# Kernel tuning notes

Hardware: AMD Instinct MI355X
Metric: run time of the kernel (lower is better)

Reference implementation:

```python
import jax, jax.numpy as jnp
import numpy as np

N, E, D, G, L = 100000, 1600000, 64, 512, 3
EPS = 1e-5


def setup_inputs() -> dict:
    key = jax.random.key(0)
    ks = jax.random.split(key, 8)
    x = jax.random.normal(ks[0], (N, D), dtype=jnp.float32)
    edge_index = jax.random.randint(ks[1], (2, E), 0, N, dtype=jnp.int32)
    batch = jnp.sort(jax.random.randint(ks[2], (N,), 0, G, dtype=jnp.int32))
    s = 1.0 / np.sqrt(D)
    convW = jax.random.normal(ks[3], (L, D, D), dtype=jnp.float32) * s
    convB = jnp.zeros((L, D), jnp.float32)
    bn_g = jnp.ones((L, D), jnp.float32); bn_b = jnp.zeros((L, D), jnp.float32)
    ln_g = jnp.ones((L, D), jnp.float32); ln_b = jnp.zeros((L, D), jnp.float32)
    W1 = jax.random.normal(ks[4], (3 * D, 2 * D), dtype=jnp.float32) * (1.0 / np.sqrt(3 * D))
    b1 = jnp.zeros((2 * D,), jnp.float32)
    ln1_g = jnp.ones((2 * D,), jnp.float32); ln1_b = jnp.zeros((2 * D,), jnp.float32)
    W2 = jax.random.normal(ks[5], (2 * D, D), dtype=jnp.float32) * (1.0 / np.sqrt(2 * D))
    b2 = jnp.zeros((D,), jnp.float32)
    ln2_g = jnp.ones((D,), jnp.float32); ln2_b = jnp.zeros((D,), jnp.float32)
    W3 = jax.random.normal(ks[6], (D, 1), dtype=jnp.float32) * s
    b3 = jnp.zeros((1,), jnp.float32)
    return dict(x=x, edge_index=edge_index, batch=batch, convW=convW, convB=convB,
                bn_g=bn_g, bn_b=bn_b, ln_g=ln_g, ln_b=ln_b,
                W1=W1, b1=b1, ln1_g=ln1_g, ln1_b=ln1_b,
                W2=W2, b2=b2, ln2_g=ln2_g, ln2_b=ln2_b, W3=W3, b3=b3)


def _layer_norm(h, g, b):
    mu = jnp.mean(h, axis=-1, keepdims=True)
    var = jnp.mean((h - mu) ** 2, axis=-1, keepdims=True)
    return (h - mu) * jax.lax.rsqrt(var + EPS) * g + b


def _forward(x, edge_index, batch, convW, convB, bn_g, bn_b, ln_g, ln_b,
             W1, b1, ln1_g, ln1_b, W2, b2, ln2_g, ln2_b, W3, b3):
    n = x.shape[0]
    loops = jnp.arange(n, dtype=edge_index.dtype)
    src = jnp.concatenate([edge_index[0], loops])  # self-loops as in GCNConv
    dst = jnp.concatenate([edge_index[1], loops])
    deg = jax.ops.segment_sum(jnp.ones_like(src, dtype=x.dtype), dst, num_segments=n)
    dinv = jnp.where(deg > 0, jax.lax.rsqrt(deg), 0.0)
    norm = (dinv[src] * dinv[dst])[:, None]  # [E+N, 1]

    h = x
    for i in range(L):
        x_in = h
        hw = h @ convW[i]                                   # [N, D]
        agg = jax.ops.segment_sum(norm * hw[src], dst, num_segments=n) + convB[i]
        # BatchNorm1d (train-mode batch stats, biased var)
        mu = jnp.mean(agg, axis=0)
        var = jnp.mean((agg - mu) ** 2, axis=0)
        hb = (agg - mu) * jax.lax.rsqrt(var + EPS) * bn_g[i] + bn_b[i]
        if i > 0:
            hb = hb + x_in  # residual (shapes match: D == D)
        h = jax.nn.gelu(_layer_norm(hb, ln_g[i], ln_b[i]), approximate=False)

    # multi-pool over graphs
    cnt = jax.ops.segment_sum(jnp.ones((n,), x.dtype), batch, num_segments=G)[:, None]
    s = jax.ops.segment_sum(h, batch, num_segments=G)
    mean = s / jnp.maximum(cnt, 1.0)
    mx = jax.ops.segment_max(h, batch, num_segments=G)
    mx = jnp.where(cnt > 0, mx, 0.0)
    z = jnp.concatenate([mean, mx, s], axis=1)  # [G, 3D]

    z = jax.nn.gelu(_layer_norm(z @ W1 + b1, ln1_g, ln1_b), approximate=False)
    z = jax.nn.gelu(_layer_norm(z @ W2 + b2, ln2_g, ln2_b), approximate=False)
    return z @ W3 + b3  # [G, num_classes]


def reference(x, edge_index, batch, convW, convB, bn_g, bn_b, ln_g, ln_b,
              W1, b1, ln1_g, ln1_b, W2, b2, ln2_g, ln2_b, W3, b3):
    return _forward(x, edge_index, batch, convW, convB, bn_g, bn_b, ln_g, ln_b,
                    W1, b1, ln1_g, ln1_b, W2, b2, ln2_g, ln2_b, W3, b3)
```

## Files before the change

kernel.cpp:

```cpp
#include <hip/hip_runtime.h>
#include <hip/hip_bf16.h>
#include <hip/hip_fp16.h>

#define DD 64
#define EPSV 1e-5f
#define NSLICE 16

typedef __attribute__((ext_vector_type(4))) _Float16 f16x4;
typedef __attribute__((ext_vector_type(8))) _Float16 f16x8;
typedef __attribute__((ext_vector_type(4))) float f32x4;

static __device__ __forceinline__ float fatomic_add(float* p, float v) {
#if defined(__HIP_DEVICE_COMPILE__)
    return unsafeAtomicAdd(p, v);
#else
    return 0.f;
#endif
}

static __device__ __forceinline__ float gelu_exact(float x) {
    return 0.5f * x * (1.0f + erff(x * 0.70710678118654752f));
}

static __device__ __forceinline__ void acc_u4(float* a8, uint4 v) {
    const __half2* hp = reinterpret_cast<const __half2*>(&v);
#pragma unroll
    for (int p = 0; p < 4; ++p) {
        float2 f = __half22float2(hp[p]);
        a8[2 * p] += f.x;
        a8[2 * p + 1] += f.y;
    }
}

__global__ void k_hist(const int* __restrict__ dst, int* __restrict__ counts, int e) {
    int i = blockIdx.x * 256 + threadIdx.x;
    if (i < e) atomicAdd(&counts[dst[i]], 1);
}

__global__ __launch_bounds__(1024) void k_bsum(const int* __restrict__ counts,
                                               int* __restrict__ bsum, int n) {
    __shared__ int wsum[16];
    int t = threadIdx.x;
    int i = blockIdx.x * 1024 + t;
    int v = (i < n) ? counts[i] : 0;
    int lane = t & 63, wv = t >> 6;
    int x = v;
#pragma unroll
    for (int o = 1; o < 64; o <<= 1) x += __shfl_xor(x, o, 64);
    if (lane == 0) wsum[wv] = x;
    __syncthreads();
    if (t == 0) {
        int r = 0;
#pragma unroll
        for (int w = 0; w < 16; ++w) r += wsum[w];
        bsum[blockIdx.x] = r;
    }
}

__global__ __launch_bounds__(128) void k_bscan(int* __restrict__ bsum, int nb) {
    __shared__ int ws[2];
    int t = threadIdx.x;
    int lane = t & 63, wv = t >> 6;
    int v = (t < nb) ? bsum[t] : 0;
    int x = v;
#pragma unroll
    for (int o = 1; o < 64; o <<= 1) {
        int u = __shfl_up(x, o, 64);
        if (lane >= o) x += u;
    }
    if (lane == 63) ws[wv] = x;
    __syncthreads();
    int add = (wv == 1) ? ws[0] : 0;
    if (t < nb) bsum[t] = add + x - v;
}

__global__ __launch_bounds__(1024) void k_downsweep(const int* __restrict__ counts,
                                                    const int* __restrict__ bsum,
                                                    int* __restrict__ off,
                                                    float* __restrict__ dinv,
                                                    int* __restrict__ bcur,
                                                    int n, int etotal) {
    __shared__ int wsum[16];
    int t = threadIdx.x;
    int i = blockIdx.x * 1024 + t;
    int v = (i < n) ? counts[i] : 0;
    int lane = t & 63, wv = t >> 6;
    int x = v;
#pragma unroll
    for (int o = 1; o < 64; o <<= 1) {
        int u = __shfl_up(x, o, 64);
        if (lane >= o) x += u;
    }
    if (lane == 63) wsum[wv] = x;
    __syncthreads();
    if (t == 0) {
        int r = 0;
#pragma unroll
        for (int w = 0; w < 16; ++w) { int y = wsum[w]; wsum[w] = r; r += y; }
    }
    __syncthreads();
    if (i < n) {
        int excl = bsum[blockIdx.x] + wsum[wv] + x - v;
        off[i] = excl;
        dinv[i] = rsqrtf((float)v + 1.0f);
        if ((i & 255) == 0) bcur[i >> 8] = excl;
        if (i == n - 1) off[n] = etotal;
    }
}

__global__ __launch_bounds__(1024) void k_dhist(const int* __restrict__ off,
                                                int* __restrict__ dcount, int n) {
    __shared__ int h[256];
    int t = threadIdx.x;
    if (t < 256) h[t] = 0;
    __syncthreads();
    int i = blockIdx.x * 1024 + t;
    if (i < n) {
        int d = min(off[i + 1] - off[i], 255);
        atomicAdd(&h[d], 1);
    }
    __syncthreads();
    if (t < 256 && h[t]) atomicAdd(&dcount[t], h[t]);
}

__global__ __launch_bounds__(256) void k_dscan(const int* __restrict__ dcount,
                                               int* __restrict__ dcur) {
    __shared__ int ws[4];
    int t = threadIdx.x;
    int lane = t & 63, wv = t >> 6;
    int v = dcount[t];
    int x = v;
#pragma unroll
    for (int o = 1; o < 64; o <<= 1) {
        int u = __shfl_up(x, o, 64);
        if (lane >= o) x += u;
    }
    if (lane == 63) ws[wv] = x;
    __syncthreads();
    int add = 0;
    for (int w = 0; w < wv; ++w) add += ws[w];
    dcur[t] = add + x - v;
}

__global__ __launch_bounds__(1024) void k_dscatter(const int* __restrict__ off,
                                                   int* __restrict__ dcur,
                                                   int* __restrict__ perm, int n) {
    __shared__ int lcnt[256], lbase[256];
    int t = threadIdx.x;
    if (t < 256) lcnt[t] = 0;
    __syncthreads();
    int i = blockIdx.x * 1024 + t;
    int d = 0, rank = 0;
    if (i < n) {
        d = min(off[i + 1] - off[i], 255);
        rank = atomicAdd(&lcnt[d], 1);
    }
    __syncthreads();
    if (t < 256 && lcnt[t]) lbase[t] = atomicAdd(&dcur[t], lcnt[t]);
    __syncthreads();
    if (i < n) perm[lbase[d] + rank] = i;
}

#define ACHUNK 2048
#define NBMAX 400
__global__ __launch_bounds__(256) void k_binA(const int* __restrict__ src,
                                              const int* __restrict__ dst,
                                              int* __restrict__ ebuf,
                                              int* __restrict__ bcur,
                                              int e, int nbuck) {
    __shared__ int cnt[NBMAX], startb[NBMAX], posb[NBMAX], gbase[NBMAX];
    __shared__ int stage[ACHUNK];
    __shared__ unsigned short stb[ACHUNK];
    int t = threadIdx.x;
    for (int cbase = blockIdx.x * ACHUNK; cbase < e; cbase += gridDim.x * ACHUNK) {
        int cval = min(ACHUNK, e - cbase);
        for (int i = t; i < nbuck; i += 256) { cnt[i] = 0; posb[i] = 0; }
        __syncthreads();
        int eb[8], es[8];
#pragma unroll
        for (int k = 0; k < 8; ++k) {
            int i = t + k * 256;
            if (i < cval) {
                int s = src[cbase + i];
                int d = dst[cbase + i];
                eb[k] = d >> 8;
                es[k] = s | ((d & 255) << 24);
                atomicAdd(&cnt[eb[k]], 1);
            } else eb[k] = -1;
        }
        __syncthreads();
        if (t == 0) {
            int r = 0;
            for (int b2 = 0; b2 < nbuck; ++b2) { startb[b2] = r; r += cnt[b2]; }
        }
        __syncthreads();
        for (int i = t; i < nbuck; i += 256)
            if (cnt[i] > 0) gbase[i] = atomicAdd(&bcur[i], cnt[i]);
#pragma unroll
        for (int k = 0; k < 8; ++k)
            if (eb[k] >= 0) {
                int idx = startb[eb[k]] + atomicAdd(&posb[eb[k]], 1);
                stage[idx] = es[k];
                stb[idx] = (unsigned short)eb[k];
            }
        __syncthreads();
        for (int i = t; i < cval; i += 256) {
            int b2 = stb[i];
            ebuf[gbase[b2] + (i - startb[b2])] = stage[i];
        }
        __syncthreads();
    }
}

__global__ __launch_bounds__(256) void k_binB(const int* __restrict__ ebuf,
                                              const int* __restrict__ offs,
                                              int* __restrict__ csr, int n) {
    __shared__ int cur[256];
    int b = blockIdx.x;
    int base = b << 8;
    int nn = min(256, n - base);
    int t = threadIdx.x;
    if (t < nn) cur[t] = offs[base + t];
    __syncthreads();
    int e0 = offs[base], e1 = offs[base + nn];
    for (int i = e0 + t; i < e1; i += 256) {
        int packed = ebuf[i];
        int dl = ((unsigned)packed) >> 24;
        int pos = atomicAdd(&cur[dl], 1);
        csr[pos] = packed & 0x00FFFFFF;
    }
}

__global__ void k_misc(const float* __restrict__ x, const float* __restrict__ dinv,
                       __half* __restrict__ mA, __half* __restrict__ mB, int n,
                       const int* __restrict__ batch, int* __restrict__ bnd, int g) {
    int i = blockIdx.x * 256 + threadIdx.x;
    int total = n * 64;
    if (i < total) {
        mA[i] = __float2half_rn(x[i] * dinv[i >> 6]);
    } else if (i < total + 64) {
        mA[i] = __float2half_rn(0.f);
        mB[i] = __float2half_rn(0.f);
    }
    if (i < n) {
        int b = batch[i];
        if (i == 0)
            for (int q = 0; q <= b; ++q) bnd[q] = 0;
        else {
            int pb = batch[i - 1];
            for (int q = pb + 1; q <= b; ++q) bnd[q] = i;
        }
        if (i == n - 1)
            for (int q = b + 1; q <= g; ++q) bnd[q] = n;
    }
}

__global__ __launch_bounds__(256, 4) void k_gather_gemm(const int* __restrict__ off,
                                                        const int* __restrict__ csr,
                                                        const float* __restrict__ dinv,
                                                        const __half* __restrict__ m16,
                                                        const float* __restrict__ W,
                                                        const float* __restrict__ convB,
                                                        const int* __restrict__ perm,
                                                        float* __restrict__ agg,
                                                        float* __restrict__ gstat,
                                                        int n, int nzero) {
    __shared__ float sred[128];
    const int t = threadIdx.x;
    const int lane = t & 63, wv = t >> 6;
    const int g = lane >> 4, ln = lane & 15;

    f16x8 bfr[2][4];
#pragma unroll
    for (int kt = 0; kt < 2; ++kt)
#pragma unroll
        for (int nt = 0; nt < 4; ++nt) {
            f16x8 h;
#pragma unroll
            for (int j = 0; j < 8; ++j)
                h[j] = (_Float16)W[(32 * kt + 8 * g + j) * 64 + 16 * nt + ln];
            bfr[kt][nt] = h;
        }

    if (t < 128) sred[t] = 0.f;
    __syncthreads();

    const int ntiles = (n + 15) >> 4;
    const int tile = blockIdx.x * 4 + wv;
    float s_acc[4] = {0.f, 0.f, 0.f, 0.f}, q_acc[4] = {0.f, 0.f, 0.f, 0.f};

    if (tile < ntiles) {
        const int slot = tile * 16 + ln;
        const bool valid = slot < n;
        const int node = valid ? perm[slot] : -1;
        const int row_self = valid ? node : nzero;
        int a = 0, deg = 0;
        float dd = 0.f;
        if (valid) {
            a = off[node];
            deg = off[node + 1] - a;
            dd = dinv[node];
        }
        int md = deg;
#pragma unroll
        for (int o = 1; o < 64; o <<= 1) md = max(md, __shfl_xor(md, o, 64));

        float acc[2][8];
#pragma unroll
        for (int kt = 0; kt < 2; ++kt)
#pragma unroll
            for (int j = 0; j < 8; ++j) acc[kt][j] = 0.f;

        const uint4* mrow4 = (const uint4*)m16;
        {
            const uint4* rp = mrow4 + ((size_t)row_self << 3) + g;
            uint4 v0 = rp[0], v1 = rp[4];
            acc_u4(acc[0], v0);
            acc_u4(acc[1], v1);
        }
        int ecur[4];
#pragma unroll
        for (int k = 0; k < 4; ++k) ecur[k] = (k < deg) ? csr[a + k] : nzero;
        for (int i = 0; i < md; i += 4) {
            int enx[4];
#pragma unroll
            for (int k = 0; k < 4; ++k) enx[k] = (i + 4 + k < deg) ? csr[a + i + 4 + k] : nzero;
            uint4 v[4][2];
#pragma unroll
            for (int r = 0; r < 4; ++r) {
                const uint4* rp = mrow4 + ((size_t)ecur[r] << 3) + g;
                v[r][0] = rp[0];
                v[r][1] = rp[4];
            }
#pragma unroll
            for (int r = 0; r < 4; ++r) {
                acc_u4(acc[0], v[r][0]);
                acc_u4(acc[1], v[r][1]);
            }
#pragma unroll
            for (int k = 0; k < 4; ++k) ecur[k] = enx[k];
        }

        f32x4 c[4];
#pragma unroll
        for (int nt = 0; nt < 4; ++nt) c[nt] = (f32x4){0.f, 0.f, 0.f, 0.f};
#pragma unroll
        for (int kt = 0; kt < 2; ++kt) {
            f16x8 ah, ar;
#pragma unroll
            for (int j = 0; j < 8; ++j) {
                float v = acc[kt][j] * dd;
                _Float16 h = (_Float16)v;
                ah[j] = h;
                ar[j] = (_Float16)(v - (float)h);
            }
#pragma unroll
            for (int nt = 0; nt < 4; ++nt) {
                c[nt] = __builtin_amdgcn_mfma_f32_16x16x32_f16(ah, bfr[kt][nt], c[nt], 0, 0, 0);
                c[nt] = __builtin_amdgcn_mfma_f32_16x16x32_f16(ar, bfr[kt][nt], c[nt], 0, 0, 0);
            }
        }

        int prow[4];
#pragma unroll
        for (int i = 0; i < 4; ++i) prow[i] = __shfl(node, 4 * g + i, 64);
        const float bias[4] = {convB[ln], convB[16 + ln], convB[32 + ln], convB[48 + ln]};
#pragma unroll
        for (int nt = 0; nt < 4; ++nt) {
#pragma unroll
            for (int i = 0; i < 4; ++i) {
                if (prow[i] >= 0) {
                    float v = c[nt][i] + bias[nt];
                    agg[(size_t)prow[i] * 64 + 16 * nt + ln] = v;
                    s_acc[nt] += v;
                    q_acc[nt] += v * v;
                }
            }
        }
#pragma unroll
        for (int nt = 0; nt < 4; ++nt) {
            s_acc[nt] += __shfl_xor(s_acc[nt], 16, 64);
            s_acc[nt] += __shfl_xor(s_acc[nt], 32, 64);
            q_acc[nt] += __shfl_xor(q_acc[nt], 16, 64);
            q_acc[nt] += __shfl_xor(q_acc[nt], 32, 64);
        }
        if (g == 0) {
#pragma unroll
            for (int nt = 0; nt < 4; ++nt) {
                atomicAdd(&sred[16 * nt + ln], s_acc[nt]);
                atomicAdd(&sred[64 + 16 * nt + ln], q_acc[nt]);
            }
        }
    }
    __syncthreads();
    if (t < 64) {
        float* gs = gstat + (blockIdx.x & (NSLICE - 1)) * 128;
        fatomic_add(&gs[t], sred[t]);
        fatomic_add(&gs[64 + t], sred[64 + t]);
    }
}

__global__ __launch_bounds__(256) void k_bn_ln_gelu(const float* __restrict__ agg,
                                                    const __half* __restrict__ m16res,
                                                    const float* __restrict__ gstat,
                                                    const float* __restrict__ dinv,
                                                    const float* __restrict__ bng,
                                                    const float* __restrict__ bnb,
                                                    const float* __restrict__ lng,
                                                    const float* __restrict__ lnb,
                                                    __half* __restrict__ m16out,
                                                    int n, int has_res, int scale_out) {
    int t = threadIdx.x;
    int lane = t & 63, wv = t >> 6;
    float fs = 0.f, fq = 0.f;
#pragma unroll
    for (int s = 0; s < NSLICE; ++s) {
        fs += gstat[s * 128 + lane];
        fq += gstat[s * 128 + 64 + lane];
    }
    float invN = 1.0f / (float)n;
    float mu_c = fs * invN;
    float var_c = fq * invN - mu_c * mu_c;
    float bscale = rsqrtf(var_c + EPSV) * bng[lane];
    float bshift = bnb[lane];
    float lg = lng[lane], lb = lnb[lane];
    for (int r = blockIdx.x * 4 + wv; r < n; r += gridDim.x * 4) {
        float dd = dinv[r];
        float x = agg[(size_t)r * 64 + lane];
        float hb = (x - mu_c) * bscale + bshift;
        if (has_res) hb += __half2float(m16res[(size_t)r * 64 + lane]) * (1.0f / dd);
        float ssum = hb;
#pragma unroll
        for (int off = 32; off; off >>= 1) ssum += __shfl_xor(ssum, off, 64);
        float rmu = ssum * (1.f / 64.f);
        float d = hb - rmu;
        float vs = d * d;
#pragma unroll
        for (int off = 32; off; off >>= 1) vs += __shfl_xor(vs, off, 64);
        float rvar = vs * (1.f / 64.f);
        float ln = d * rsqrtf(rvar + EPSV) * lg + lb;
        float g = gelu_exact(ln);
        float outv = scale_out ? g * dd : g;
        m16out[(size_t)r * 64 + lane] = __float2half_rn(outv);
    }
}

__global__ __launch_bounds__(256) void k_pool_z(const __half* __restrict__ h,
                                                const int* __restrict__ bnd,
                                                float* __restrict__ z) {
    int g = blockIdx.x;
    int t = threadIdx.x;
    int lane = t & 63, wv = t >> 6;
    int s0 = bnd[g], e0 = bnd[g + 1];
    float s = 0.f, mx = -INFINITY;
    for (int i = s0 + wv; i < e0; i += 4) {
        float v = __half2float(h[(size_t)i * 64 + lane]);
        s += v;
        mx = fmaxf(mx, v);
    }
    __shared__ float ss[256], sm[256];
    ss[t] = s;
    sm[t] = mx;
    __syncthreads();
    if (t < 64) {
        float fs = ss[t] + ss[t + 64] + ss[t + 128] + ss[t + 192];
        float fm = fmaxf(fmaxf(sm[t], sm[t + 64]), fmaxf(sm[t + 128], sm[t + 192]));
        float cntf = (float)(e0 - s0);
        float mean = fs / fmaxf(cntf, 1.0f);
        if (e0 == s0) fm = 0.f;
        z[g * 192 + t] = mean;
        z[g * 192 + 64 + t] = fm;
        z[g * 192 + 128 + t] = fs;
    }
}

__global__ __launch_bounds__(128) void k_head(const float* __restrict__ z,
                                              const float* __restrict__ W1, const float* __restrict__ b1,
                                              const float* __restrict__ ln1g, const float* __restrict__ ln1b,
                                              const float* __restrict__ W2, const float* __restrict__ b2,
                                              const float* __restrict__ ln2g, const float* __restrict__ ln2b,
                                              const float* __restrict__ W3, const float* __restrict__ b3,
                                              float* __restrict__ out) {
    int g = blockIdx.x;
    int t = threadIdx.x;
    int lane = t & 63, wv = t >> 6;
    __shared__ float zl[192], h1[128], red[2];
    for (int i = t; i < 192; i += 128) zl[i] = z[g * 192 + i];
    __syncthreads();
    float acc = b1[t];
    for (int k = 0; k < 192; ++k) acc += zl[k] * W1[k * 128 + t];
    float s = acc;
#pragma unroll
    for (int off = 32; off; off >>= 1) s += __shfl_xor(s, off, 64);
    if (lane == 0) red[wv] = s;
    __syncthreads();
    float mu = (red[0] + red[1]) * (1.f / 128.f);
    float d = acc - mu;
    float q = d * d;
#pragma unroll
    for (int off = 32; off; off >>= 1) q += __shfl_xor(q, off, 64);
    __syncthreads();
    if (lane == 0) red[wv] = q;
    __syncthreads();
    float var = (red[0] + red[1]) * (1.f / 128.f);
    float ln = d * rsqrtf(var + EPSV) * ln1g[t] + ln1b[t];
    h1[t] = gelu_exact(ln);
    __syncthreads();
    if (t < 64) {
        float acc2 = b2[t];
        for (int k = 0; k < 128; ++k) acc2 += h1[k] * W2[k * 64 + t];
        float s2 = acc2;
#pragma unroll
        for (int off = 32; off; off >>= 1) s2 += __shfl_xor(s2, off, 64);
        float mu2 = s2 * (1.f / 64.f);
        float d2 = acc2 - mu2;
        float q2 = d2 * d2;
#pragma unroll
        for (int off = 32; off; off >>= 1) q2 += __shfl_xor(q2, off, 64);
        float var2 = q2 * (1.f / 64.f);
        float l2 = d2 * rsqrtf(var2 + EPSV) * ln2g[t] + ln2b[t];
        float g2 = gelu_exact(l2);
        float p = g2 * W3[t];
#pragma unroll
        for (int off = 32; off; off >>= 1) p += __shfl_xor(p, off, 64);
        if (t == 0) out[g] = p + b3[0];
    }
}

extern "C" void kernel_launch(void* const* d_in, const int* in_sizes, int n_in,
                              void* d_out, int out_size, void* d_ws, size_t ws_size,
                              hipStream_t stream) {
    const float* x      = (const float*)d_in[0];
    const int*   eidx   = (const int*)d_in[1];
    const int*   batch  = (const int*)d_in[2];
    const float* convW  = (const float*)d_in[3];
    const float* convB  = (const float*)d_in[4];
    const float* bn_g   = (const float*)d_in[5];
    const float* bn_b   = (const float*)d_in[6];
    const float* ln_g   = (const float*)d_in[7];
    const float* ln_b   = (const float*)d_in[8];
    const float* W1     = (const float*)d_in[9];
    const float* b1     = (const float*)d_in[10];
    const float* ln1g   = (const float*)d_in[11];
    const float* ln1b   = (const float*)d_in[12];
    const float* W2     = (const float*)d_in[13];
    const float* b2     = (const float*)d_in[14];
    const float* ln2g   = (const float*)d_in[15];
    const float* ln2b   = (const float*)d_in[16];
    const float* W3     = (const float*)d_in[17];
    const float* b3     = (const float*)d_in[18];
    float* out = (float*)d_out;

    const int N = in_sizes[0] / DD;
    const int E = in_sizes[1] / 2;
    const int G = out_size;
    const int* esrc = eidx;
    const int* edst = eidx + E;

    char* ws = (char*)d_ws;
    size_t off_b = 0;
    auto alloc = [&](size_t bytes) {
        size_t p = off_b;
        off_b = (off_b + bytes + 255) & ~(size_t)255;
        return (void*)(ws + p);
    };
    int*    offs   = (int*)alloc((size_t)(N + 1) * 4);
    float*  dinv   = (float*)alloc((size_t)N * 4);
    int*    csr    = (int*)alloc((size_t)E * 4);
    int*    ebuf   = (int*)alloc((size_t)E * 4);
    __half* m16A   = (__half*)alloc((size_t)(N + 1) * DD * 2);
    __half* m16B   = (__half*)alloc((size_t)(N + 1) * DD * 2);
    float*  aggbuf = (float*)alloc((size_t)N * DD * 4);
    float*  gstats = (float*)alloc((size_t)3 * NSLICE * 128 * 4);
    int*    perm   = (int*)alloc((size_t)N * 4);
    int*    dcount = (int*)alloc(256 * 4);
    int*    dcur   = (int*)alloc(256 * 4);
    int*    bnd    = (int*)alloc((size_t)(G + 1) * 4);
    int*    bsum   = (int*)alloc(((size_t)(N + 1023) / 1024) * 4);
    int*    bcur   = (int*)alloc(((size_t)(N + 255) / 256) * 4);
    int*   counts = (int*)aggbuf;
    float* z      = aggbuf;
    (void)ws_size; (void)n_in;

    const int nb = (N + 1023) / 1024;
    const int nbuck = (N + 255) / 256;

    hipMemsetAsync(counts, 0, (size_t)N * 4, stream);
    hipMemsetAsync(gstats, 0, (size_t)3 * NSLICE * 128 * 4, stream);
    hipMemsetAsync(dcount, 0, 256 * 4, stream);
    k_hist<<<(E + 255) / 256, 256, 0, stream>>>(edst, counts, E);
    k_bsum<<<nb, 1024, 0, stream>>>(counts, bsum, N);
    k_bscan<<<1, 128, 0, stream>>>(bsum, nb);
    k_downsweep<<<nb, 1024, 0, stream>>>(counts, bsum, offs, dinv, bcur, N, E);
    k_dhist<<<nb, 1024, 0, stream>>>(offs, dcount, N);
    k_dscan<<<1, 256, 0, stream>>>(dcount, dcur);
    k_dscatter<<<nb, 1024, 0, stream>>>(offs, dcur, perm, N);
    k_binA<<<(E + ACHUNK - 1) / ACHUNK, 256, 0, stream>>>(esrc, edst, ebuf, bcur, E, nbuck);
    k_binB<<<nbuck, 256, 0, stream>>>(ebuf, offs, csr, N);
    k_misc<<<((N + 1) * DD + 255) / 256, 256, 0, stream>>>(x, dinv, m16A, m16B, N, batch, bnd, G);

    __half* gin[3]  = {m16A, m16B, m16A};
    __half* gout[3] = {m16B, m16A, m16B};

    const int ntiles = (N + 15) / 16;
    const int gblocks = (ntiles + 3) / 4;

    for (int l = 0; l < 3; ++l) {
        float* gstat = gstats + (size_t)l * NSLICE * 128;
        k_gather_gemm<<<gblocks, 256, 0, stream>>>(offs, csr, dinv, (const __half*)gin[l],
                                                   convW + (size_t)l * DD * DD, convB + l * DD,
                                                   perm, aggbuf, gstat, N, N);
        k_bn_ln_gelu<<<2048, 256, 0, stream>>>(aggbuf, gin[l], gstat, dinv,
                                               bn_g + l * DD, bn_b + l * DD,
                                               ln_g + l * DD, ln_b + l * DD,
                                               gout[l], N, l > 0 ? 1 : 0, l < 2 ? 1 : 0);
    }

    k_pool_z<<<G, 256, 0, stream>>>(m16B, bnd, z);
    k_head<<<G, 128, 0, stream>>>(z, W1, b1, ln1g, ln1b, W2, b2, ln2g, ln2b, W3, b3, out);
}
```

Baseline: 476.6 us.

## Build CSR from bucket-level counts and compute per-node offsets inside binB

Replaces the per-node global degree histogram with a bucket-level histogram done in shared memory, followed by a single-block scan over buckets. Per-node offsets and dinv are now computed inside k_binB with a local count and scan over each bucket's edges. This removes the N-sized memset, the 1.6M global atomics on node counters and two scan kernels. The cost is an extra pass over ebuf in binB, and the degree-sort kernels are moved after binB because they depend on offs.

```diff
diff --git a/kernel.cpp b/kernel.cpp
--- a/kernel.cpp
+++ b/kernel.cpp
@@ -32,36 +32,35 @@
     }
 }
 
-__global__ void k_hist(const int* __restrict__ dst, int* __restrict__ counts, int e) {
-    int i = blockIdx.x * 256 + threadIdx.x;
-    if (i < e) atomicAdd(&counts[dst[i]], 1);
-}
-
-__global__ __launch_bounds__(1024) void k_bsum(const int* __restrict__ counts,
-                                               int* __restrict__ bsum, int n) {
-    __shared__ int wsum[16];
-    int t = threadIdx.x;
-    int i = blockIdx.x * 1024 + t;
-    int v = (i < n) ? counts[i] : 0;
-    int lane = t & 63, wv = t >> 6;
-    int x = v;
-#pragma unroll
-    for (int o = 1; o < 64; o <<= 1) x += __shfl_xor(x, o, 64);
-    if (lane == 0) wsum[wv] = x;
-    __syncthreads();
-    if (t == 0) {
-        int r = 0;
-#pragma unroll
-        for (int w = 0; w < 16; ++w) r += wsum[w];
-        bsum[blockIdx.x] = r;
-    }
-}
-
-__global__ __launch_bounds__(128) void k_bscan(int* __restrict__ bsum, int nb) {
-    __shared__ int ws[2];
-    int t = threadIdx.x;
-    int lane = t & 63, wv = t >> 6;
-    int v = (t < nb) ? bsum[t] : 0;
+#define ACHUNK 2048
+#define NBMAX 400
+
+__global__ __launch_bounds__(1024) void k_bcount(const int* __restrict__ dst,
+                                                 int* __restrict__ bucketCnt,
+                                                 int e, int nbuck) {
+    __shared__ int h[NBMAX];
+    int t = threadIdx.x;
+    for (int i = t; i < nbuck; i += 1024) h[i] = 0;
+    __syncthreads();
+    int base = blockIdx.x * 8192;
+#pragma unroll
+    for (int k = 0; k < 8; ++k) {
+        int i = base + k * 1024 + t;
+        if (i < e) atomicAdd(&h[dst[i] >> 8], 1);
+    }
+    __syncthreads();
+    for (int i = t; i < nbuck; i += 1024)
+        if (h[i]) atomicAdd(&bucketCnt[i], h[i]);
+}
+
+__global__ __launch_bounds__(512) void k_bscan2(const int* __restrict__ bucketCnt,
+                                                int* __restrict__ bbase,
+                                                int* __restrict__ bcur,
+                                                int* __restrict__ offs,
+                                                int nbuck, int etotal, int n) {
+    __shared__ int ws[8];
+    int t = threadIdx.x, lane = t & 63, wv = t >> 6;
+    int v = (t < nbuck) ? bucketCnt[t] : 0;
     int x = v;
 #pragma unroll
     for (int o = 1; o < 64; o <<= 1) {
@@ -70,41 +69,16 @@
     }
     if (lane == 63) ws[wv] = x;
     __syncthreads();
-    int add = (wv == 1) ? ws[0] : 0;
-    if (t < nb) bsum[t] = add + x - v;
-}
-
-__global__ __launch_bounds__(1024) void k_downsweep(const int* __restrict__ counts,
-                                                    const int* __restrict__ bsum,
-                                                    int* __restrict__ off,
-                                                    float* __restrict__ dinv,
-                                                    int* __restrict__ bcur,
-                                                    int n, int etotal) {
-    __shared__ int wsum[16];
-    int t = threadIdx.x;
-    int i = blockIdx.x * 1024 + t;
-    int v = (i < n) ? counts[i] : 0;
-    int lane = t & 63, wv = t >> 6;
-    int x = v;
-#pragma unroll
-    for (int o = 1; o < 64; o <<= 1) {
-        int u = __shfl_up(x, o, 64);
-        if (lane >= o) x += u;
-    }
-    if (lane == 63) wsum[wv] = x;
-    __syncthreads();
+    int add = 0;
+    for (int w = 0; w < wv; ++w) add += ws[w];
+    int excl = add + x - v;
+    if (t < nbuck) {
+        bbase[t] = excl;
+        bcur[t] = excl;
+    }
     if (t == 0) {
-        int r = 0;
-#pragma unroll
-        for (int w = 0; w < 16; ++w) { int y = wsum[w]; wsum[w] = r; r += y; }
-    }
-    __syncthreads();
-    if (i < n) {
-        int excl = bsum[blockIdx.x] + wsum[wv] + x - v;
-        off[i] = excl;
-        dinv[i] = rsqrtf((float)v + 1.0f);
-        if ((i & 255) == 0) bcur[i >> 8] = excl;
-        if (i == n - 1) off[n] = etotal;
+        bbase[nbuck] = etotal;
+        offs[n] = etotal;
     }
 }
 
@@ -161,8 +135,6 @@
     if (i < n) perm[lbase[d] + rank] = i;
 }
 
-#define ACHUNK 2048
-#define NBMAX 400
 __global__ __launch_bounds__(256) void k_binA(const int* __restrict__ src,
                                               const int* __restrict__ dst,
                                               int* __restrict__ ebuf,
@@ -213,16 +185,40 @@
 }
 
 __global__ __launch_bounds__(256) void k_binB(const int* __restrict__ ebuf,
-                                              const int* __restrict__ offs,
+                                              const int* __restrict__ bbase,
+                                              int* __restrict__ offs,
+                                              float* __restrict__ dinv,
                                               int* __restrict__ csr, int n) {
-    __shared__ int cur[256];
+    __shared__ int cnt[256], cur[256], ws[4];
     int b = blockIdx.x;
     int base = b << 8;
     int nn = min(256, n - base);
     int t = threadIdx.x;
-    if (t < nn) cur[t] = offs[base + t];
-    __syncthreads();
-    int e0 = offs[base], e1 = offs[base + nn];
+    int e0 = bbase[b], e1 = bbase[b + 1];
+    cnt[t] = 0;
+    __syncthreads();
+    for (int i = e0 + t; i < e1; i += 256)
+        atomicAdd(&cnt[((unsigned)ebuf[i]) >> 24], 1);
+    __syncthreads();
+    int v = cnt[t];
+    int lane = t & 63, wv = t >> 6;
+    int x = v;
+#pragma unroll
+    for (int o = 1; o < 64; o <<= 1) {
+        int u = __shfl_up(x, o, 64);
+        if (lane >= o) x += u;
+    }
+    if (lane == 63) ws[wv] = x;
+    __syncthreads();
+    int add = 0;
+    for (int w = 0; w < wv; ++w) add += ws[w];
+    int excl = add + x - v;
+    if (t < nn) {
+        offs[base + t] = e0 + excl;
+        dinv[base + t] = rsqrtf((float)v + 1.0f);
+    }
+    cur[t] = e0 + excl;
+    __syncthreads();
     for (int i = e0 + t; i < e1; i += 256) {
         int packed = ebuf[i];
         int dl = ((unsigned)packed) >> 24;
@@ -576,27 +572,25 @@
     int*    dcount = (int*)alloc(256 * 4);
     int*    dcur   = (int*)alloc(256 * 4);
     int*    bnd    = (int*)alloc((size_t)(G + 1) * 4);
-    int*    bsum   = (int*)alloc(((size_t)(N + 1023) / 1024) * 4);
+    int*    bucketCnt = (int*)alloc((size_t)NBMAX * 4);
+    int*    bbase  = (int*)alloc((size_t)(NBMAX + 1) * 4);
     int*    bcur   = (int*)alloc(((size_t)(N + 255) / 256) * 4);
-    int*   counts = (int*)aggbuf;
-    float* z      = aggbuf;
+    float* z = aggbuf;
     (void)ws_size; (void)n_in;
 
+    const int nbuck = (N + 255) / 256;
     const int nb = (N + 1023) / 1024;
-    const int nbuck = (N + 255) / 256;
-
-    hipMemsetAsync(counts, 0, (size_t)N * 4, stream);
+
     hipMemsetAsync(gstats, 0, (size_t)3 * NSLICE * 128 * 4, stream);
     hipMemsetAsync(dcount, 0, 256 * 4, stream);
-    k_hist<<<(E + 255) / 256, 256, 0, stream>>>(edst, counts, E);
-    k_bsum<<<nb, 1024, 0, stream>>>(counts, bsum, N);
-    k_bscan<<<1, 128, 0, stream>>>(bsum, nb);
-    k_downsweep<<<nb, 1024, 0, stream>>>(counts, bsum, offs, dinv, bcur, N, E);
+    hipMemsetAsync(bucketCnt, 0, (size_t)NBMAX * 4, stream);
+    k_bcount<<<(E + 8191) / 8192, 1024, 0, stream>>>(edst, bucketCnt, E, nbuck);
+    k_bscan2<<<1, 512, 0, stream>>>(bucketCnt, bbase, bcur, offs, nbuck, E, N);
+    k_binA<<<(E + ACHUNK - 1) / ACHUNK, 256, 0, stream>>>(esrc, edst, ebuf, bcur, E, nbuck);
+    k_binB<<<nbuck, 256, 0, stream>>>(ebuf, bbase, offs, dinv, csr, N);
     k_dhist<<<nb, 1024, 0, stream>>>(offs, dcount, N);
     k_dscan<<<1, 256, 0, stream>>>(dcount, dcur);
     k_dscatter<<<nb, 1024, 0, stream>>>(offs, dcur, perm, N);
-    k_binA<<<(E + ACHUNK - 1) / ACHUNK, 256, 0, stream>>>(esrc, edst, ebuf, bcur, E, nbuck);
-    k_binB<<<nbuck, 256, 0, stream>>>(ebuf, offs, csr, N);
     k_misc<<<((N + 1) * DD + 255) / 256, 256, 0, stream>>>(x, dinv, m16A, m16B, N, batch, bnd, G);
 
     __half* gin[3]  = {m16A, m16B, m16A};
```

After: 418.6 us. 12.2% less time.
